# Optimization experiments

Measured on AMD Instinct MI355X. Metric: run time of the kernel, lower is better.

Reference implementation:

```python
import jax, jax.numpy as jnp
import numpy as np

B, L, D = 32, 1024, 256
G = 3 * D


def _gelu(x):
    return jax.nn.gelu(x, approximate=False)


def _start_embed(x, w0, b0, w1, b1, w2, b2):
    out = x @ w0.T + b0
    res = out
    out = _gelu(out)
    out = _gelu(out @ w1.T + b1)
    out = out @ w2.T + b2
    return out + res


def _gru_layer(x_seq, h0, w_ih, w_hh, b_ih, b_hh):
    # x_seq: [L, B, in]; torch GRU gate order: r, z, n
    xp = jnp.einsum('lbi,gi->lbg', x_seq, w_ih) + b_ih  # [L, B, 3D]
    def step(h, xpt):
        hp = h @ w_hh.T + b_hh
        xr, xz, xn = jnp.split(xpt, 3, axis=-1)
        hr, hz, hn = jnp.split(hp, 3, axis=-1)
        r = jax.nn.sigmoid(xr + hr)
        z = jax.nn.sigmoid(xz + hz)
        n = jnp.tanh(xn + r * hn)
        h_new = (1.0 - z) * n + z * h
        return h_new, h_new
    _, outs = jax.lax.scan(step, h0, xp)
    return outs  # [L, B, D]


def _p(k, shape):
    return jax.random.normal(k, shape, jnp.float32) * 0.05


def setup_inputs():
    key = jax.random.key(0)
    ks = iter(jax.random.split(key, 32))
    inp = {}
    inp['noisy_enc'] = jax.random.normal(next(ks), (B, L), jnp.float32)
    inp['mask'] = jnp.ones((B, L), jnp.float32)
    inp['trg_seq'] = jax.random.randint(next(ks), (B, L), 0, 2)
    inp['se_w0'] = _p(next(ks), (D, L)); inp['se_b0'] = _p(next(ks), (D,))
    inp['se_w1'] = _p(next(ks), (D, D)); inp['se_b1'] = _p(next(ks), (D,))
    inp['se_w2'] = _p(next(ks), (D, D)); inp['se_b2'] = _p(next(ks), (D,))
    inp['w_ih0'] = _p(next(ks), (G, 1)); inp['w_hh0'] = _p(next(ks), (G, D))
    inp['b_ih0'] = _p(next(ks), (G,));   inp['b_hh0'] = _p(next(ks), (G,))
    inp['w_ih1'] = _p(next(ks), (G, D)); inp['w_hh1'] = _p(next(ks), (G, D))
    inp['b_ih1'] = _p(next(ks), (G,));   inp['b_hh1'] = _p(next(ks), (G,))
    inp['attn_w1'] = _p(next(ks), (D, D)); inp['attn_b1'] = _p(next(ks), (D,))
    inp['comb_w'] = _p(next(ks), (D, 3 * D)); inp['comb_b'] = _p(next(ks), (D,))
    inp['dec_w0'] = _p(next(ks), (D, D)); inp['dec_b0'] = _p(next(ks), (D,))
    inp['dec_w1'] = _p(next(ks), (D, D)); inp['dec_b1'] = _p(next(ks), (D,))
    inp['dec_w2'] = _p(next(ks), (1, D)); inp['dec_b2'] = _p(next(ks), (1,))
    return inp


def reference(noisy_enc, mask, trg_seq,
              se_w0, se_b0, se_w1, se_b1, se_w2, se_b2,
              w_ih0, w_hh0, b_ih0, b_hh0, w_ih1, w_hh1, b_ih1, b_hh1,
              attn_w1, attn_b1, comb_w, comb_b,
              dec_w0, dec_b0, dec_w1, dec_b1, dec_w2, dec_b2):
    # shift target right, prepend start token = 1
    trg = jnp.concatenate(
        [jnp.ones((B, 1), jnp.float32), trg_seq[:, :-1].astype(jnp.float32)], axis=-1)
    x = trg.T[:, :, None]  # [L, B, 1]

    sh = _start_embed(noisy_enc, se_w0, se_b0, se_w1, se_b1, se_w2, se_b2)  # [B, D]
    o0 = _gru_layer(x, sh, w_ih0, w_hh0, b_ih0, b_hh0)
    o1 = _gru_layer(o0, sh, w_ih1, w_hh1, b_ih1, b_hh1)
    outs = jnp.transpose(o1, (1, 0, 2))  # [B, L, D]

    # causal dot-product attention (diagonal masked out, row 0 zeroed)
    modif = outs @ attn_w1.T + attn_b1
    attn_logits = jnp.einsum('bld,bmd->blm', outs, modif)
    causal = jnp.triu(jnp.full((L, L), -1e16, jnp.float32))
    attn = jax.nn.softmax(attn_logits + causal, axis=-1)
    attn = attn * (jnp.arange(L) > 0).astype(attn.dtype)[None, :, None]
    ctx = jnp.einsum('blm,bmd->bld', attn, outs)

    sh_b = jnp.broadcast_to(sh[:, None, :], (B, L, D))
    cat = jnp.concatenate([ctx, outs, sh_b], axis=-1)  # [B, L, 3D]
    dec = jnp.tanh(cat @ comb_w.T + comb_b)
    h = _gelu(dec @ dec_w0.T + dec_b0)
    h = _gelu(h @ dec_w1.T + dec_b1)
    logits = h @ dec_w2.T + dec_b2  # [B, L, 1]

    p = jax.nn.sigmoid(logits)
    output = jnp.concatenate([1.0 - p, p], axis=-1)  # [B, L, 2]
    decoded_msg_bits = jnp.sign(logits)
    return (output, decoded_msg_bits, mask, logits)
```

## Files before the change

kernel.cpp:

```cpp
#include <hip/hip_runtime.h>
#include <math.h>

#define NROWS 32768

typedef float v4 __attribute__((ext_vector_type(4)));
typedef _Float16 h2 __attribute__((ext_vector_type(2)));
typedef _Float16 f16x8 __attribute__((ext_vector_type(8)));
typedef float f32x4 __attribute__((ext_vector_type(4)));

__device__ __forceinline__ float geluf(float x){ return 0.5f*x*(1.0f+erff(x*0.70710678118654752f)); }

__device__ __forceinline__ float fexp2(float x){
#if __has_builtin(__builtin_amdgcn_exp2f)
    return __builtin_amdgcn_exp2f(x);
#else
    return exp2f(x);
#endif
}
__device__ __forceinline__ float frcp(float x){
#if __has_builtin(__builtin_amdgcn_rcpf)
    return __builtin_amdgcn_rcpf(x);
#else
    return 1.0f/x;
#endif
}
#define LOG2E 1.44269504088896f
__device__ __forceinline__ float fexp(float x){ return fexp2(x*LOG2E); }
__device__ __forceinline__ float sigm(float x){ return frcp(1.0f + fexp2(-LOG2E*x)); }
__device__ __forceinline__ float ftanh(float x){ return 1.0f - 2.0f*frcp(fexp2(2.0f*LOG2E*x) + 1.0f); }

__device__ __forceinline__ float dot2(h2 a, h2 b, float c){
#if __has_builtin(__builtin_amdgcn_fdot2)
    return __builtin_amdgcn_fdot2(a, b, c, false);
#else
    return c + (float)a.x*(float)b.x + (float)a.y*(float)b.y;
#endif
}
__device__ __forceinline__ h2 cvt2(float2 a){ return h2{(_Float16)a.x, (_Float16)a.y}; }

__device__ __forceinline__ void wg_barrier(){
    asm volatile("s_waitcnt lgkmcnt(0)" ::: "memory");
    __builtin_amdgcn_s_barrier();
    __builtin_amdgcn_sched_barrier(0);
}

__global__ __launch_bounds__(256) void k_start_embed(
    const float* __restrict__ ne, const float* __restrict__ w0, const float* __restrict__ b0,
    const float* __restrict__ w1, const float* __restrict__ b1,
    const float* __restrict__ w2, const float* __restrict__ b2,
    float* __restrict__ sh)
{
    __shared__ __align__(16) float encL[1024];
    __shared__ __align__(16) float g1[256];
    __shared__ __align__(16) float g2[256];
    int b = blockIdx.x, t = threadIdx.x;
    for (int i = t; i < 1024; i += 256) encL[i] = ne[b*1024 + i];
    __syncthreads();
    const float4* wr = (const float4*)(w0 + (size_t)t*1024);
    const float4* e4 = (const float4*)encL;
    float a0=0,a1=0,a2=0,a3=0;
    #pragma unroll 8
    for (int k = 0; k < 256; ++k){ float4 w = wr[k], e = e4[k];
        a0 += w.x*e.x; a1 += w.y*e.y; a2 += w.z*e.z; a3 += w.w*e.w; }
    float t1 = a0+a1+a2+a3 + b0[t];
    float res = t1;
    g1[t] = geluf(t1);
    __syncthreads();
    const float4* w1r = (const float4*)(w1 + (size_t)t*256);
    const float4* g14 = (const float4*)g1;
    a0=a1=a2=a3=0.f;
    #pragma unroll 8
    for (int k = 0; k < 64; ++k){ float4 w = w1r[k], e = g14[k];
        a0 += w.x*e.x; a1 += w.y*e.y; a2 += w.z*e.z; a3 += w.w*e.w; }
    g2[t] = geluf(a0+a1+a2+a3 + b1[t]);
    __syncthreads();
    const float4* w2r = (const float4*)(w2 + (size_t)t*256);
    const float4* g24 = (const float4*)g2;
    a0=a1=a2=a3=0.f;
    #pragma unroll 8
    for (int k = 0; k < 64; ++k){ float4 w = w2r[k], e = g24[k];
        a0 += w.x*e.x; a1 += w.y*e.y; a2 += w.z*e.z; a3 += w.w*e.w; }
    sh[b*256 + t] = a0+a1+a2+a3 + b2[t] + res;
}

__device__ __forceinline__ int hperm(int dim){
    return ((dim >> 3) & 7)*32 + ((dim >> 6) << 3) + (dim & 7);
}

template<int LAYER>
__global__ __launch_bounds__(512) void k_gru3(
    const float* __restrict__ w_hh, const float* __restrict__ b_hh,
    const float* __restrict__ w_ih0, const float* __restrict__ b_ih0,
    const float* __restrict__ xp1,
    const int*   __restrict__ trg,
    const float* __restrict__ sh,
    float* __restrict__ out)
{
    __shared__ __align__(16) float4 wNs[8192];
    __shared__ __align__(16) _Float16 hbuf[2][256];
    __shared__ __align__(16) float bitL[1024];
    int b = blockIdx.x, t = threadIdx.x;
    int d = t >> 1, half = t & 1;

    if (LAYER == 0) {
        #pragma unroll
        for (int i = 0; i < 2; ++i) {
            int idx = t + i*512;
            bitL[idx] = (idx == 0) ? 1.0f : (float)trg[b*1024 + idx - 1];
        }
    }

    {
        const float2* src = (const float2*)(w_hh + (size_t)(512 + d)*256 + half*128);
        #pragma unroll
        for (int kk = 0; kk < 16; ++kk) {
            h2 p0 = cvt2(src[kk*4+0]), p1 = cvt2(src[kk*4+1]);
            h2 p2 = cvt2(src[kk*4+2]), p3 = cvt2(src[kk*4+3]);
            float4 v;
            v.x = __builtin_bit_cast(float, p0); v.y = __builtin_bit_cast(float, p1);
            v.z = __builtin_bit_cast(float, p2); v.w = __builtin_bit_cast(float, p3);
            wNs[kk*512 + t] = v;
        }
    }
    h2 wR[64], wZ[64];
    {
        const float2* wr = (const float2*)(w_hh + (size_t)d*256       + half*128);
        const float2* wz = (const float2*)(w_hh + (size_t)(d+256)*256 + half*128);
        #pragma unroll
        for (int k = 0; k < 64; ++k) { wR[k] = cvt2(wr[k]); wZ[k] = cvt2(wz[k]); }
    }
    float bhr = b_hh[d], bhz = b_hh[256 + d], bhn = b_hh[512 + d];
    float wir=0.f, wiz=0.f, win=0.f, bir=0.f, biz=0.f, bin=0.f;
    if (LAYER == 0) {
        wir = w_ih0[d]; wiz = w_ih0[256 + d]; win = w_ih0[512 + d];
        bir = b_ih0[d]; biz = b_ih0[256 + d]; bin = b_ih0[512 + d];
    }

    float hreg = sh[b*256 + d];
    if (half == 0) hbuf[0][hperm(d)] = (_Float16)hreg;

    float xr = 0.f, xz = 0.f, xn = 0.f;
    if (LAYER == 1) {
        size_t base = (size_t)b*768;
        xr = xp1[base + d]; xz = xp1[base + 256 + d]; xn = xp1[base + 512 + d];
    }
    __syncthreads();

    for (int l = 0; l < 1024; ++l) {
        const float4* hb4 = (const float4*)(&hbuf[l & 1][0]);
        float ar = 0.f, az = 0.f, an = 0.f;
        #pragma unroll
        for (int kk = 0; kk < 16; ++kk) {
            float4 hv = hb4[(kk & 7)*4 + half*2 + (kk >> 3)];
            float4 wv = wNs[kk*512 + t];
            h2 h0 = __builtin_bit_cast(h2, hv.x);
            h2 h1 = __builtin_bit_cast(h2, hv.y);
            h2 hc = __builtin_bit_cast(h2, hv.z);
            h2 h3 = __builtin_bit_cast(h2, hv.w);
            ar = dot2(wR[4*kk+0], h0, ar); ar = dot2(wR[4*kk+1], h1, ar);
            ar = dot2(wR[4*kk+2], hc, ar); ar = dot2(wR[4*kk+3], h3, ar);
            az = dot2(wZ[4*kk+0], h0, az); az = dot2(wZ[4*kk+1], h1, az);
            az = dot2(wZ[4*kk+2], hc, az); az = dot2(wZ[4*kk+3], h3, az);
            an = dot2(__builtin_bit_cast(h2, wv.x), h0, an);
            an = dot2(__builtin_bit_cast(h2, wv.y), h1, an);
            an = dot2(__builtin_bit_cast(h2, wv.z), hc, an);
            an = dot2(__builtin_bit_cast(h2, wv.w), h3, an);
        }
        ar += __shfl_xor(ar, 1);
        az += __shfl_xor(az, 1);
        an += __shfl_xor(an, 1);
        if (LAYER == 0) {
            float bit = bitL[l];
            xr = bir + bit*wir; xz = biz + bit*wiz; xn = bin + bit*win;
        }
        float r = sigm(xr + ar + bhr);
        float z = sigm(xz + az + bhz);
        float n = ftanh(xn + r*(an + bhn));
        hreg = (1.0f - z)*n + z*hreg;
        if (half == 0) {
            hbuf[(l + 1) & 1][hperm(d)] = (_Float16)hreg;
        } else {
            size_t oidx = (LAYER == 0) ? (((size_t)l*32 + b)*256 + d)
                                       : (((size_t)b*1024 + l)*256 + d);
            out[oidx] = hreg;
        }
        if (LAYER == 1) {
            int ln = (l < 1023) ? (l + 1) : 1023;
            size_t base = ((size_t)ln*32 + b)*768;
            xr = xp1[base + d]; xz = xp1[base + 256 + d]; xn = xp1[base + 512 + d];
        }
        wg_barrier();
    }
}

__global__ __launch_bounds__(256, 3) void k_gemm_mfma(
    const float* __restrict__ A, const float* __restrict__ B,
    const float* __restrict__ bias, float* __restrict__ C,
    int M, int N, int K, int act, int aMode,
    const float* __restrict__ A1, const float* __restrict__ A2)
{
    __shared__ __align__(16) _Float16 As[128][40];
    __shared__ __align__(16) _Float16 Bs[128][40];
    int nbn = N >> 7;
    int bx = blockIdx.x % nbn, by = blockIdx.x / nbn;
    int m0 = by << 7, n0 = bx << 7;
    int t = threadIdx.x;
    int w = t >> 6, l = t & 63;
    int wm = w >> 1, wn = w & 1;
    int lc = l & 15, lg = l >> 4;
    f32x4 acc[4][4] = {};
    for (int kt = 0; kt < K; kt += 32) {
        __syncthreads();
        #pragma unroll
        for (int p = 0; p < 4; ++p) {
            int slot = t + p*256;
            int m = slot >> 3, kc = slot & 7;
            int gk = kt + kc*4;
            float4 va;
            if (aMode == 0) {
                va = *(const float4*)(A + (size_t)(m0+m)*K + gk);
            } else {
                int part = gk >> 8, kk = gk & 255;
                const float* P = (part == 0) ? A : ((part == 1) ? A1 : A2);
                int row = (part == 2) ? ((m0+m) >> 10) : (m0+m);
                va = *(const float4*)(P + (size_t)row*256 + kk);
            }
            h2 pa; pa[0] = (_Float16)va.x; pa[1] = (_Float16)va.y;
            h2 pb; pb[0] = (_Float16)va.z; pb[1] = (_Float16)va.w;
            *(float2*)(&As[m][kc*4]) = make_float2(__builtin_bit_cast(float, pa),
                                                   __builtin_bit_cast(float, pb));
            float4 vb = *(const float4*)(B + (size_t)(n0+m)*K + gk);
            h2 qa; qa[0] = (_Float16)vb.x; qa[1] = (_Float16)vb.y;
            h2 qb; qb[0] = (_Float16)vb.z; qb[1] = (_Float16)vb.w;
            *(float2*)(&Bs[m][kc*4]) = make_float2(__builtin_bit_cast(float, qa),
                                                   __builtin_bit_cast(float, qb));
        }
        __syncthreads();
        f16x8 af[4], bf[4];
        #pragma unroll
        for (int mt = 0; mt < 4; ++mt)
            af[mt] = *(const f16x8*)(&As[wm*64 + mt*16 + lc][lg*8]);
        #pragma unroll
        for (int nt = 0; nt < 4; ++nt)
            bf[nt] = *(const f16x8*)(&Bs[wn*64 + nt*16 + lc][lg*8]);
        #pragma unroll
        for (int mt = 0; mt < 4; ++mt)
            #pragma unroll
            for (int nt = 0; nt < 4; ++nt)
                acc[mt][nt] = __builtin_amdgcn_mfma_f32_16x16x32_f16(af[mt], bf[nt], acc[mt][nt], 0, 0, 0);
    }
    #pragma unroll
    for (int nt = 0; nt < 4; ++nt) {
        int col = n0 + wn*64 + nt*16 + lc;
        float bv = bias[col];
        #pragma unroll
        for (int mt = 0; mt < 4; ++mt) {
            int rbase = m0 + wm*64 + mt*16 + lg*4;
            #pragma unroll
            for (int r = 0; r < 4; ++r) {
                float v = acc[mt][nt][r] + bv;
                if (act == 1) v = geluf(v);
                else if (act == 2) v = ftanh(v);
                C[(size_t)(rbase + r)*N + col] = v;
            }
        }
    }
}

__global__ __launch_bounds__(256) void k_attn(
    const float* __restrict__ outs, const float* __restrict__ modif, float* __restrict__ ctx)
{
    __shared__ __align__(16) float Qs[16][256];
    __shared__ __align__(16) float KVs[32][256];
    __shared__ __align__(16) float sS[16][32];
    __shared__ float rowScaleL[16];
    __shared__ float rowLL[16];
    int b = blockIdx.y, l0 = blockIdx.x << 4, t = threadIdx.x;
    for (int idx = t; idx < 1024; idx += 256) {
        int r = idx >> 6, k4 = idx & 63;
        *(float4*)&Qs[r][k4*4] = *(const float4*)(outs + ((size_t)b*1024 + l0 + r)*256 + k4*4);
    }
    int sr = t >> 4, sj = t & 15;
    int rp = t >> 5, cg = t & 31;
    float rowM = -1e30f, rowL = 0.f;
    float accA[8] = {}, accB[8] = {};
    int nt = ((l0 + 14) >> 5) + 1;
    for (int tt = 0; tt < nt; ++tt) {
        int m0 = tt << 5;
        __syncthreads();
        for (int idx = t; idx < 2048; idx += 256) {
            int mm = idx >> 6, k4 = idx & 63;
            *(float4*)&KVs[mm][k4*4] = *(const float4*)(modif + ((size_t)b*1024 + m0 + mm)*256 + k4*4);
        }
        __syncthreads();
        {
            int mp = sj << 1;
            const float4* q4 = (const float4*)Qs[sr];
            const float4* x4 = (const float4*)KVs[mp];
            const float4* y4 = (const float4*)KVs[mp+1];
            float s0 = 0.f, s1 = 0.f;
            #pragma unroll 8
            for (int kk = 0; kk < 64; ++kk) {
                int k = (kk + sj) & 63;
                float4 q = q4[k], x = x4[k], y = y4[k];
                s0 += q.x*x.x + q.y*x.y + q.z*x.z + q.w*x.w;
                s1 += q.x*y.x + q.y*y.y + q.z*y.z + q.w*y.w;
            }
            int l = l0 + sr;
            if (m0 + mp     >= l) s0 = -1e30f;
            if (m0 + mp + 1 >= l) s1 = -1e30f;
            sS[sr][mp] = s0; sS[sr][mp+1] = s1;
        }
        __syncthreads();
        {
            float v0 = sS[sr][sj], v1 = sS[sr][sj+16];
            float mx = fmaxf(v0, v1);
            for (int off = 8; off; off >>= 1) mx = fmaxf(mx, __shfl_xor(mx, off));
            float newM = fmaxf(rowM, mx);
            float scale, p0, p1;
            if (newM < -1e29f) { scale = 1.f; p0 = 0.f; p1 = 0.f; }
            else { scale = fexp(rowM - newM); p0 = fexp(v0 - newM); p1 = fexp(v1 - newM); }
            rowM = newM;
            float ts = p0 + p1;
            for (int off = 8; off; off >>= 1) ts += __shfl_xor(ts, off);
            rowL = rowL*scale + ts;
            sS[sr][sj] = p0; sS[sr][sj+16] = p1;
            if (sj == 0) { rowScaleL[sr] = scale; rowLL[sr] = rowL; }
        }
        __syncthreads();
        for (int idx = t; idx < 2048; idx += 256) {
            int mm = idx >> 6, k4 = idx & 63;
            *(float4*)&KVs[mm][k4*4] = *(const float4*)(outs + ((size_t)b*1024 + m0 + mm)*256 + k4*4);
        }
        __syncthreads();
        {
            float sc0 = rowScaleL[2*rp], sc1 = rowScaleL[2*rp+1];
            #pragma unroll
            for (int j = 0; j < 8; ++j) { accA[j] *= sc0; accB[j] *= sc1; }
            int c0 = cg << 3;
            #pragma unroll 4
            for (int mm = 0; mm < 32; ++mm) {
                float p0 = sS[2*rp][mm], p1 = sS[2*rp+1][mm];
                float4 vA = *(const float4*)&KVs[mm][c0];
                float4 vB = *(const float4*)&KVs[mm][c0+4];
                accA[0] += p0*vA.x; accA[1] += p0*vA.y; accA[2] += p0*vA.z; accA[3] += p0*vA.w;
                accA[4] += p0*vB.x; accA[5] += p0*vB.y; accA[6] += p0*vB.z; accA[7] += p0*vB.w;
                accB[0] += p1*vA.x; accB[1] += p1*vA.y; accB[2] += p1*vA.z; accB[3] += p1*vA.w;
                accB[4] += p1*vB.x; accB[5] += p1*vB.y; accB[6] += p1*vB.z; accB[7] += p1*vB.w;
            }
        }
    }
    __syncthreads();
    int c0 = cg << 3;
    {
        int l = l0 + 2*rp;
        float inv = (l == 0) ? 0.f : 1.f/rowLL[2*rp];
        float4* cp = (float4*)(ctx + ((size_t)b*1024 + l)*256 + c0);
        cp[0] = make_float4(accA[0]*inv, accA[1]*inv, accA[2]*inv, accA[3]*inv);
        cp[1] = make_float4(accA[4]*inv, accA[5]*inv, accA[6]*inv, accA[7]*inv);
    }
    {
        int l = l0 + 2*rp + 1;
        float inv = 1.f/rowLL[2*rp+1];
        float4* cp = (float4*)(ctx + ((size_t)b*1024 + l)*256 + c0);
        cp[0] = make_float4(accB[0]*inv, accB[1]*inv, accB[2]*inv, accB[3]*inv);
        cp[1] = make_float4(accB[4]*inv, accB[5]*inv, accB[6]*inv, accB[7]*inv);
    }
}

__global__ __launch_bounds__(256) void k_final(
    const float* __restrict__ h2v, const float* __restrict__ w2, const float* __restrict__ b2,
    const float* __restrict__ mask, float* __restrict__ out)
{
    int i = blockIdx.x*256 + threadIdx.x;
    const float4* h4 = (const float4*)(h2v + (size_t)i*256);
    const float4* w4 = (const float4*)w2;
    float a0=0,a1=0,a2=0,a3=0;
    #pragma unroll 8
    for (int k = 0; k < 64; ++k) {
        float4 h = h4[k], w = w4[k];
        a0 += h.x*w.x; a1 += h.y*w.y; a2 += h.z*w.z; a3 += h.w*w.w;
    }
    float lg = a0+a1+a2+a3 + b2[0];
    float p = sigm(lg);
    out[2*i]     = 1.0f - p;
    out[2*i + 1] = p;
    out[65536  + i] = (lg > 0.f) ? 1.0f : ((lg < 0.f) ? -1.0f : 0.0f);
    out[98304  + i] = mask[i];
    out[131072 + i] = lg;
}

extern "C" void kernel_launch(void* const* d_in, const int* in_sizes, int n_in,
                              void* d_out, int out_size, void* d_ws, size_t ws_size,
                              hipStream_t stream)
{
    const float* ne      = (const float*)d_in[0];
    const float* mask    = (const float*)d_in[1];
    const int*   trg     = (const int*)  d_in[2];
    const float* se_w0   = (const float*)d_in[3];
    const float* se_b0   = (const float*)d_in[4];
    const float* se_w1   = (const float*)d_in[5];
    const float* se_b1   = (const float*)d_in[6];
    const float* se_w2   = (const float*)d_in[7];
    const float* se_b2   = (const float*)d_in[8];
    const float* w_ih0   = (const float*)d_in[9];
    const float* w_hh0   = (const float*)d_in[10];
    const float* b_ih0   = (const float*)d_in[11];
    const float* b_hh0   = (const float*)d_in[12];
    const float* w_ih1   = (const float*)d_in[13];
    const float* w_hh1   = (const float*)d_in[14];
    const float* b_ih1   = (const float*)d_in[15];
    const float* b_hh1   = (const float*)d_in[16];
    const float* attn_w1 = (const float*)d_in[17];
    const float* attn_b1 = (const float*)d_in[18];
    const float* comb_w  = (const float*)d_in[19];
    const float* comb_b  = (const float*)d_in[20];
    const float* dec_w0  = (const float*)d_in[21];
    const float* dec_b0  = (const float*)d_in[22];
    const float* dec_w1  = (const float*)d_in[23];
    const float* dec_b1  = (const float*)d_in[24];
    const float* dec_w2  = (const float*)d_in[25];
    const float* dec_b2  = (const float*)d_in[26];

    float* W    = (float*)d_ws;
    float* sh   = W;
    float* o0   = W + 8192;
    float* xp1  = W + 8396800;
    float* outs = W + 33562624;
    float* modif = o0;
    float* ctx  = xp1;
    float* dec  = xp1 + 8388608;
    float* h1   = xp1 + 16777216;
    float* h2b  = o0;
    float* out  = (float*)d_out;

    k_start_embed<<<32, 256, 0, stream>>>(ne, se_w0, se_b0, se_w1, se_b1, se_w2, se_b2, sh);
    k_gru3<0><<<32, 512, 0, stream>>>(w_hh0, b_hh0, w_ih0, b_ih0, nullptr, trg, sh, o0);
    k_gemm_mfma<<<1536, 256, 0, stream>>>(o0, w_ih1, b_ih1, xp1, NROWS, 768, 256, 0, 0, nullptr, nullptr);
    k_gru3<1><<<32, 512, 0, stream>>>(w_hh1, b_hh1, nullptr, nullptr, xp1, trg, sh, outs);
    k_gemm_mfma<<<512, 256, 0, stream>>>(outs, attn_w1, attn_b1, modif, NROWS, 256, 256, 0, 0, nullptr, nullptr);
    { dim3 ag(64, 32); k_attn<<<ag, 256, 0, stream>>>(outs, modif, ctx); }
    k_gemm_mfma<<<512, 256, 0, stream>>>(ctx, comb_w, comb_b, dec, NROWS, 256, 768, 2, 3, outs, sh);
    k_gemm_mfma<<<512, 256, 0, stream>>>(dec, dec_w0, dec_b0, h1, NROWS, 256, 256, 1, 0, nullptr, nullptr);
    k_gemm_mfma<<<512, 256, 0, stream>>>(h1, dec_w1, dec_b1, h2b, NROWS, 256, 256, 1, 0, nullptr, nullptr);
    k_final<<<128, 256, 0, stream>>>(h2b, dec_w2, dec_b2, mask, out);
}
```

Before: 3.435 ms.

## Rewrite causal attention with split-fp16 MFMA and 64-row query tiles

Replaces the scalar FP32 flash-style attention kernel with one that runs QK^T and PV on 16x16x32 fp16 MFMA instructions. FP32 accuracy is approximated by splitting each operand into high and low fp16 parts, which takes three MFMAs per product. Query tiles grow from 16 to 64 rows per block with one wave per interleaved row set, and V is stored transposed in LDS. This trades FP32 ALU work for matrix-core throughput, at the cost of conversion work, larger LDS use, scalar transposed LDS stores and fewer blocks.

```diff
diff --git a/kernel.cpp b/kernel.cpp
--- a/kernel.cpp
+++ b/kernel.cpp
@@ -267,104 +267,137 @@
     }
 }
 
-__global__ __launch_bounds__(256) void k_attn(
+__global__ __launch_bounds__(256) void k_attn_mfma(
     const float* __restrict__ outs, const float* __restrict__ modif, float* __restrict__ ctx)
 {
-    __shared__ __align__(16) float Qs[16][256];
-    __shared__ __align__(16) float KVs[32][256];
-    __shared__ __align__(16) float sS[16][32];
-    __shared__ float rowScaleL[16];
-    __shared__ float rowLL[16];
-    int b = blockIdx.y, l0 = blockIdx.x << 4, t = threadIdx.x;
-    for (int idx = t; idx < 1024; idx += 256) {
-        int r = idx >> 6, k4 = idx & 63;
-        *(float4*)&Qs[r][k4*4] = *(const float4*)(outs + ((size_t)b*1024 + l0 + r)*256 + k4*4);
-    }
-    int sr = t >> 4, sj = t & 15;
-    int rp = t >> 5, cg = t & 31;
-    float rowM = -1e30f, rowL = 0.f;
-    float accA[8] = {}, accB[8] = {};
-    int nt = ((l0 + 14) >> 5) + 1;
-    for (int tt = 0; tt < nt; ++tt) {
+    __shared__ __align__(16) _Float16 Qsh[64][264];
+    __shared__ __align__(16) _Float16 Qsl[64][264];
+    __shared__ __align__(16) _Float16 Ksh[32][264];
+    __shared__ __align__(16) _Float16 Ksl[32][264];
+    __shared__ __align__(16) _Float16 Vth[256][40];
+    __shared__ __align__(16) _Float16 Vtl[256][40];
+    __shared__ __align__(16) _Float16 sPh[4][16][40];
+    __shared__ __align__(16) _Float16 sPl[4][16][40];
+    int b = blockIdx.y, bx = blockIdx.x, l0 = bx << 6, t = threadIdx.x;
+    int w = t >> 6, l = t & 63;
+    int lc = l & 15, lg = l >> 4;
+
+    #pragma unroll
+    for (int p = 0; p < 16; ++p) {
+        int i = p*256 + t;
+        int row = i >> 6, c4 = i & 63;
+        float4 v = *(const float4*)(outs + ((size_t)b*1024 + l0 + row)*256 + c4*4);
+        _Float16 hx = (_Float16)v.x, hy = (_Float16)v.y, hz = (_Float16)v.z, hw = (_Float16)v.w;
+        h2 pa; pa[0] = hx; pa[1] = hy;
+        h2 pb; pb[0] = hz; pb[1] = hw;
+        *(float2*)(&Qsh[row][c4*4]) = make_float2(__builtin_bit_cast(float, pa),
+                                                  __builtin_bit_cast(float, pb));
+        h2 la; la[0] = (_Float16)(v.x - (float)hx); la[1] = (_Float16)(v.y - (float)hy);
+        h2 lb; lb[0] = (_Float16)(v.z - (float)hz); lb[1] = (_Float16)(v.w - (float)hw);
+        *(float2*)(&Qsl[row][c4*4]) = make_float2(__builtin_bit_cast(float, la),
+                                                  __builtin_bit_cast(float, lb));
+    }
+    __syncthreads();
+    f16x8 aqh[8], aql[8];
+    #pragma unroll
+    for (int kf = 0; kf < 8; ++kf) {
+        aqh[kf] = *(const f16x8*)(&Qsh[w + 4*lc][kf*32 + lg*8]);
+        aql[kf] = *(const f16x8*)(&Qsl[w + 4*lc][kf*32 + lg*8]);
+    }
+
+    f32x4 cacc[16] = {};
+    float rowM[4] = {-1e30f, -1e30f, -1e30f, -1e30f};
+    float rowL[4] = {0.f, 0.f, 0.f, 0.f};
+
+    int T = 2*bx + 2;
+    for (int tt = 0; tt < T; ++tt) {
         int m0 = tt << 5;
         __syncthreads();
-        for (int idx = t; idx < 2048; idx += 256) {
-            int mm = idx >> 6, k4 = idx & 63;
-            *(float4*)&KVs[mm][k4*4] = *(const float4*)(modif + ((size_t)b*1024 + m0 + mm)*256 + k4*4);
+        #pragma unroll
+        for (int p = 0; p < 8; ++p) {
+            int i = p*256 + t;
+            int row = i >> 6, c4 = i & 63;
+            float4 kv = *(const float4*)(modif + ((size_t)b*1024 + m0 + row)*256 + c4*4);
+            _Float16 hx = (_Float16)kv.x, hy = (_Float16)kv.y, hz = (_Float16)kv.z, hw = (_Float16)kv.w;
+            h2 pa; pa[0] = hx; pa[1] = hy;
+            h2 pb; pb[0] = hz; pb[1] = hw;
+            *(float2*)(&Ksh[row][c4*4]) = make_float2(__builtin_bit_cast(float, pa),
+                                                      __builtin_bit_cast(float, pb));
+            h2 la; la[0] = (_Float16)(kv.x - (float)hx); la[1] = (_Float16)(kv.y - (float)hy);
+            h2 lb; lb[0] = (_Float16)(kv.z - (float)hz); lb[1] = (_Float16)(kv.w - (float)hw);
+            *(float2*)(&Ksl[row][c4*4]) = make_float2(__builtin_bit_cast(float, la),
+                                                      __builtin_bit_cast(float, lb));
+            float4 vv = *(const float4*)(outs + ((size_t)b*1024 + m0 + row)*256 + c4*4);
+            _Float16 vx = (_Float16)vv.x, vy = (_Float16)vv.y, vz = (_Float16)vv.z, vw = (_Float16)vv.w;
+            Vth[c4*4+0][row] = vx;  Vtl[c4*4+0][row] = (_Float16)(vv.x - (float)vx);
+            Vth[c4*4+1][row] = vy;  Vtl[c4*4+1][row] = (_Float16)(vv.y - (float)vy);
+            Vth[c4*4+2][row] = vz;  Vtl[c4*4+2][row] = (_Float16)(vv.z - (float)vz);
+            Vth[c4*4+3][row] = vw;  Vtl[c4*4+3][row] = (_Float16)(vv.w - (float)vw);
         }
         __syncthreads();
-        {
-            int mp = sj << 1;
-            const float4* q4 = (const float4*)Qs[sr];
-            const float4* x4 = (const float4*)KVs[mp];
-            const float4* y4 = (const float4*)KVs[mp+1];
-            float s0 = 0.f, s1 = 0.f;
-            #pragma unroll 8
-            for (int kk = 0; kk < 64; ++kk) {
-                int k = (kk + sj) & 63;
-                float4 q = q4[k], x = x4[k], y = y4[k];
-                s0 += q.x*x.x + q.y*x.y + q.z*x.z + q.w*x.w;
-                s1 += q.x*y.x + q.y*y.y + q.z*y.z + q.w*y.w;
-            }
-            int l = l0 + sr;
-            if (m0 + mp     >= l) s0 = -1e30f;
-            if (m0 + mp + 1 >= l) s1 = -1e30f;
-            sS[sr][mp] = s0; sS[sr][mp+1] = s1;
-        }
-        __syncthreads();
-        {
-            float v0 = sS[sr][sj], v1 = sS[sr][sj+16];
+        f32x4 s0 = {0.f,0.f,0.f,0.f}, s1 = {0.f,0.f,0.f,0.f};
+        #pragma unroll
+        for (int kf = 0; kf < 8; ++kf) {
+            f16x8 b0h = *(const f16x8*)(&Ksh[lc][kf*32 + lg*8]);
+            f16x8 b0l = *(const f16x8*)(&Ksl[lc][kf*32 + lg*8]);
+            f16x8 b1h = *(const f16x8*)(&Ksh[16 + lc][kf*32 + lg*8]);
+            f16x8 b1l = *(const f16x8*)(&Ksl[16 + lc][kf*32 + lg*8]);
+            s0 = __builtin_amdgcn_mfma_f32_16x16x32_f16(aqh[kf], b0h, s0, 0, 0, 0);
+            s0 = __builtin_amdgcn_mfma_f32_16x16x32_f16(aqh[kf], b0l, s0, 0, 0, 0);
+            s0 = __builtin_amdgcn_mfma_f32_16x16x32_f16(aql[kf], b0h, s0, 0, 0, 0);
+            s1 = __builtin_amdgcn_mfma_f32_16x16x32_f16(aqh[kf], b1h, s1, 0, 0, 0);
+            s1 = __builtin_amdgcn_mfma_f32_16x16x32_f16(aqh[kf], b1l, s1, 0, 0, 0);
+            s1 = __builtin_amdgcn_mfma_f32_16x16x32_f16(aql[kf], b1h, s1, 0, 0, 0);
+        }
+        #pragma unroll
+        for (int r = 0; r < 4; ++r) {
+            int m = lg*4 + r;
+            int grow = l0 + w + 4*m;
+            float v0 = s0[r], v1 = s1[r];
+            if (m0 + lc      >= grow) v0 = -1e30f;
+            if (m0 + 16 + lc >= grow) v1 = -1e30f;
             float mx = fmaxf(v0, v1);
-            for (int off = 8; off; off >>= 1) mx = fmaxf(mx, __shfl_xor(mx, off));
-            float newM = fmaxf(rowM, mx);
-            float scale, p0, p1;
-            if (newM < -1e29f) { scale = 1.f; p0 = 0.f; p1 = 0.f; }
-            else { scale = fexp(rowM - newM); p0 = fexp(v0 - newM); p1 = fexp(v1 - newM); }
-            rowM = newM;
+            mx = fmaxf(mx, __shfl_xor(mx, 1));
+            mx = fmaxf(mx, __shfl_xor(mx, 2));
+            mx = fmaxf(mx, __shfl_xor(mx, 4));
+            mx = fmaxf(mx, __shfl_xor(mx, 8));
+            float nm = fmaxf(rowM[r], mx);
+            float sc, p0, p1;
+            if (nm < -1e29f) { sc = 1.f; p0 = 0.f; p1 = 0.f; }
+            else { sc = fexp(rowM[r] - nm); p0 = fexp(v0 - nm); p1 = fexp(v1 - nm); }
+            rowM[r] = nm;
             float ts = p0 + p1;
-            for (int off = 8; off; off >>= 1) ts += __shfl_xor(ts, off);
-            rowL = rowL*scale + ts;
-            sS[sr][sj] = p0; sS[sr][sj+16] = p1;
-            if (sj == 0) { rowScaleL[sr] = scale; rowLL[sr] = rowL; }
-        }
-        __syncthreads();
-        for (int idx = t; idx < 2048; idx += 256) {
-            int mm = idx >> 6, k4 = idx & 63;
-            *(float4*)&KVs[mm][k4*4] = *(const float4*)(outs + ((size_t)b*1024 + m0 + mm)*256 + k4*4);
-        }
-        __syncthreads();
-        {
-            float sc0 = rowScaleL[2*rp], sc1 = rowScaleL[2*rp+1];
+            ts += __shfl_xor(ts, 1);
+            ts += __shfl_xor(ts, 2);
+            ts += __shfl_xor(ts, 4);
+            ts += __shfl_xor(ts, 8);
+            rowL[r] = rowL[r]*sc + ts;
+            _Float16 p0h = (_Float16)p0, p1h = (_Float16)p1;
+            sPh[w][m][lc]      = p0h;  sPl[w][m][lc]      = (_Float16)(p0 - (float)p0h);
+            sPh[w][m][16 + lc] = p1h;  sPl[w][m][16 + lc] = (_Float16)(p1 - (float)p1h);
             #pragma unroll
-            for (int j = 0; j < 8; ++j) { accA[j] *= sc0; accB[j] *= sc1; }
-            int c0 = cg << 3;
-            #pragma unroll 4
-            for (int mm = 0; mm < 32; ++mm) {
-                float p0 = sS[2*rp][mm], p1 = sS[2*rp+1][mm];
-                float4 vA = *(const float4*)&KVs[mm][c0];
-                float4 vB = *(const float4*)&KVs[mm][c0+4];
-                accA[0] += p0*vA.x; accA[1] += p0*vA.y; accA[2] += p0*vA.z; accA[3] += p0*vA.w;
-                accA[4] += p0*vB.x; accA[5] += p0*vB.y; accA[6] += p0*vB.z; accA[7] += p0*vB.w;
-                accB[0] += p1*vA.x; accB[1] += p1*vA.y; accB[2] += p1*vA.z; accB[3] += p1*vA.w;
-                accB[4] += p1*vB.x; accB[5] += p1*vB.y; accB[6] += p1*vB.z; accB[7] += p1*vB.w;
-            }
-        }
-    }
-    __syncthreads();
-    int c0 = cg << 3;
-    {
-        int l = l0 + 2*rp;
-        float inv = (l == 0) ? 0.f : 1.f/rowLL[2*rp];
-        float4* cp = (float4*)(ctx + ((size_t)b*1024 + l)*256 + c0);
-        cp[0] = make_float4(accA[0]*inv, accA[1]*inv, accA[2]*inv, accA[3]*inv);
-        cp[1] = make_float4(accA[4]*inv, accA[5]*inv, accA[6]*inv, accA[7]*inv);
-    }
-    {
-        int l = l0 + 2*rp + 1;
-        float inv = 1.f/rowLL[2*rp+1];
-        float4* cp = (float4*)(ctx + ((size_t)b*1024 + l)*256 + c0);
-        cp[0] = make_float4(accB[0]*inv, accB[1]*inv, accB[2]*inv, accB[3]*inv);
-        cp[1] = make_float4(accB[4]*inv, accB[5]*inv, accB[6]*inv, accB[7]*inv);
+            for (int nt = 0; nt < 16; ++nt) cacc[nt][r] *= sc;
+        }
+        asm volatile("s_waitcnt lgkmcnt(0)" ::: "memory");
+        __builtin_amdgcn_sched_barrier(0);
+        f16x8 pah = *(const f16x8*)(&sPh[w][lc][lg*8]);
+        f16x8 pal = *(const f16x8*)(&sPl[w][lc][lg*8]);
+        #pragma unroll
+        for (int nt = 0; nt < 16; ++nt) {
+            f16x8 bvh = *(const f16x8*)(&Vth[nt*16 + lc][lg*8]);
+            f16x8 bvl = *(const f16x8*)(&Vtl[nt*16 + lc][lg*8]);
+            cacc[nt] = __builtin_amdgcn_mfma_f32_16x16x32_f16(pah, bvh, cacc[nt], 0, 0, 0);
+            cacc[nt] = __builtin_amdgcn_mfma_f32_16x16x32_f16(pah, bvl, cacc[nt], 0, 0, 0);
+            cacc[nt] = __builtin_amdgcn_mfma_f32_16x16x32_f16(pal, bvh, cacc[nt], 0, 0, 0);
+        }
+    }
+    #pragma unroll
+    for (int r = 0; r < 4; ++r) {
+        int grow = l0 + w + 4*(lg*4 + r);
+        float inv = (grow == 0) ? 0.f : 1.f/rowL[r];
+        #pragma unroll
+        for (int nt = 0; nt < 16; ++nt)
+            ctx[((size_t)b*1024 + grow)*256 + nt*16 + lc] = cacc[nt][r]*inv;
     }
 }
 
@@ -439,7 +472,7 @@
     k_gemm_mfma<<<1536, 256, 0, stream>>>(o0, w_ih1, b_ih1, xp1, NROWS, 768, 256, 0, 0, nullptr, nullptr);
     k_gru3<1><<<32, 512, 0, stream>>>(w_hh1, b_hh1, nullptr, nullptr, xp1, trg, sh, outs);
     k_gemm_mfma<<<512, 256, 0, stream>>>(outs, attn_w1, attn_b1, modif, NROWS, 256, 256, 0, 0, nullptr, nullptr);
-    { dim3 ag(64, 32); k_attn<<<ag, 256, 0, stream>>>(outs, modif, ctx); }
+    { dim3 ag(16, 32); k_attn_mfma<<<ag, 256, 0, stream>>>(outs, modif, ctx); }
     k_gemm_mfma<<<512, 256, 0, stream>>>(ctx, comb_w, comb_b, dec, NROWS, 256, 768, 2, 3, outs, sh);
     k_gemm_mfma<<<512, 256, 0, stream>>>(dec, dec_w0, dec_b0, h1, NROWS, 256, 256, 1, 0, nullptr, nullptr);
     k_gemm_mfma<<<512, 256, 0, stream>>>(h1, dec_w1, dec_b1, h2b, NROWS, 256, 256, 1, 0, nullptr, nullptr);
```

Measured after the change: 2.977 ms. 13.3% less time.
